# Kernel tuning notes

Hardware: AMD Instinct MI355X
Metric: run time of the kernel (lower is better)

## Reference

```python
import jax, jax.numpy as jnp
import numpy as np

NEG_SLOPE = 0.2  # LeakyReLU(0.2) used for attention scores


def setup_inputs() -> dict:
    key = jax.random.key(0)
    k1, k2, k3, k4, k5 = jax.random.split(key, 5)
    B, H, N, F, D = 1024, 32, 25, 128, 128
    return {
        "x_self": jax.random.normal(k1, (B, H, F), dtype=jnp.float32),
        "x_neigh": jax.random.normal(k2, (B, H, N, F), dtype=jnp.float32),
        "w_feat": jax.random.normal(k3, (F, D), dtype=jnp.float32) * 0.1,
        "a_self": jax.random.normal(k4, (D, 1), dtype=jnp.float32) * 0.1,
        "a_neigh": jax.random.normal(k5, (D, 1), dtype=jnp.float32) * 0.1,
    }


def reference(x_self, x_neigh, w_feat, a_self, a_neigh):
    # xw_self: [B, H, 1, D]; xw_neigh: [B, H, N, D]
    xw_self = jnp.einsum("bhf,fd->bhd", x_self, w_feat)[:, :, None, :]
    xw_neigh = jnp.einsum("bhnf,fd->bhnd", x_neigh, w_feat)
    xw_all = jnp.concatenate([xw_self, xw_neigh], axis=2)  # [B, H, N+1, D]
    # attention scores over the (self + neighbours) axis
    attn_self = jnp.einsum("bhkd,do->bhko", xw_self, a_self)   # [B, H, 1, 1]
    attn_neigh = jnp.einsum("bhkd,do->bhko", xw_all, a_neigh)  # [B, H, N+1, 1]
    attn_u = jax.nn.leaky_relu(attn_self + attn_neigh, negative_slope=NEG_SLOPE)
    attn = jax.nn.softmax(attn_u, axis=2)                      # [B, H, N+1, 1]
    h_out = jnp.sum(attn * xw_all, axis=2)                     # [B, H, D]
    return jax.nn.relu(h_out)
```

## Files before the change

kernel.cpp:

```cpp
#include <hip/hip_runtime.h>

typedef unsigned short u16;
typedef unsigned int   u32;
typedef __attribute__((ext_vector_type(4))) float f32x4;
typedef __attribute__((ext_vector_type(4))) int   i32x4;
typedef __attribute__((ext_vector_type(4))) u32   u32x4;

#define NPAIR 32768
#define NB    25
#define FD    128

__device__ __forceinline__ float bflo(u32 u){ return __uint_as_float(u << 16); }
__device__ __forceinline__ float bfhi(u32 u){ return __uint_as_float(u & 0xFFFF0000u); }
__device__ __forceinline__ u16 f2bf(float f){
  u32 u = __float_as_uint(f);
  u += 0x7FFFu + ((u >> 16) & 1u);
  return (u16)(u >> 16);
}
__device__ __forceinline__ float rowsum16(float x){
  x += __shfl_xor(x, 1);
  x += __shfl_xor(x, 2);
  x += __shfl_xor(x, 4);
  x += __shfl_xor(x, 8);
  return x;
}
__device__ __forceinline__ bool sniff_f32(const u16* __restrict__ xsniff, int l){
  const u16 v1 = xsniff[l], v2 = xsniff[64 + l];
  int e1 = (v1 >> 7) & 0xFF, e2 = (v2 >> 7) & 0xFF;
  int e = e1 > e2 ? e1 : e2;
  #pragma unroll
  for (int m = 1; m <= 32; m <<= 1){ int o = __shfl_xor(e, m); e = e > o ? e : o; }
  unsigned long long zb = __ballot(((l & 1) == 0) && (v1 == 0 || v2 == 0));
  return (e >= 141) || (__popcll(zb) >= 20);
}

__global__ __launch_bounds__(64) void prep(const void* w_, const void* as_, const void* an_,
                                           const u16* __restrict__ xsniff,
                                           float* __restrict__ wa, u16* __restrict__ wpk,
                                           int* __restrict__ flag_out){
  const int l = threadIdx.x;
  const bool isf32 = sniff_f32(xsniff, l);

  if (blockIdx.x < FD){
    const int f = blockIdx.x;
    float ps, pn;
    if (isf32){
      const float* w  = (const float*)w_;
      const float* as = (const float*)as_;
      const float* an = (const float*)an_;
      float w0 = w[f*FD + 2*l], w1 = w[f*FD + 2*l + 1];
      ps = w0*as[2*l] + w1*as[2*l+1];
      pn = w0*an[2*l] + w1*an[2*l+1];
    } else {
      const u16* w  = (const u16*)w_;
      const u16* as = (const u16*)as_;
      const u16* an = (const u16*)an_;
      u32 wd = *(const u32*)(w + f*FD + 2*l);
      u32 av = *(const u32*)(as + 2*l);
      u32 nv = *(const u32*)(an + 2*l);
      ps = bflo(wd)*bflo(av) + bfhi(wd)*bfhi(av);
      pn = bflo(wd)*bflo(nv) + bfhi(wd)*bfhi(nv);
    }
    #pragma unroll
    for(int m=1; m<=32; m<<=1){ ps += __shfl_xor(ps, m); pn += __shfl_xor(pn, m); }
    if (l == 0){ wa[f] = ps; wa[FD + f] = pn; }
    if (blockIdx.x == 0 && l == 0) flag_out[0] = isf32 ? 1 : 0;
  } else {
    const int unit = (blockIdx.x - FD)*64 + l;
    const int nt   = unit >> 8;
    const int kt   = (unit >> 6) & 3;
    const int fl   = unit & 63;
    const int col  = fl & 15, quad = fl >> 4;
    union { u16 s[8]; u32x4 u; } bb;
    #pragma unroll
    for (int j = 0; j < 8; ++j){
      const int idx = (kt*32 + quad*8 + j)*FD + nt*16 + col;
      bb.s[j] = isf32 ? f2bf(((const float*)w_)[idx]) : ((const u16*)w_)[idx];
    }
    *(u32x4*)(wpk + unit*8) = bb.u;
  }
}

template<bool FP32>
__device__ __forceinline__ void fused_body(const void* __restrict__ xs_, const void* __restrict__ xn_,
                                           const float* __restrict__ wa, const u16* __restrict__ wpk,
                                           void* __restrict__ out_, u16* __restrict__ xb){
  const int tid  = threadIdx.x;
  const int lane = tid & 63, wv = tid >> 6;
  const int g  = lane >> 4;
  const int q  = lane & 15;
  const int f0 = q << 3;
  const int pbase = blockIdx.x * 16;

  float was[8], wan[8];
  {
    f32x4 a = *(const f32x4*)(wa + f0);
    f32x4 b = *(const f32x4*)(wa + f0 + 4);
    was[0]=a[0]; was[1]=a[1]; was[2]=a[2]; was[3]=a[3];
    was[4]=b[0]; was[5]=b[1]; was[6]=b[2]; was[7]=b[3];
    f32x4 c = *(const f32x4*)(wa + FD + f0);
    f32x4 d = *(const f32x4*)(wa + FD + f0 + 4);
    wan[0]=c[0]; wan[1]=c[1]; wan[2]=c[2]; wan[3]=c[3];
    wan[4]=d[0]; wan[5]=d[1]; wan[6]=d[2]; wan[7]=d[3];
  }

  #pragma unroll 1
  for (int pp = 0; pp < 4; ++pp){
    const int row = wv*4 + pp;
    const int p   = pbase + row;

    float xf[7][8];
    #pragma unroll
    for(int i=0;i<7;++i){
      const int v = 4*i + g;
      if (v <= NB){
        if (FP32){
          const float* src = (v==0) ? ((const float*)xs_ + (size_t)p*FD + f0)
                                    : ((const float*)xn_ + (size_t)p*(NB*FD) + (size_t)(v-1)*FD + f0);
          f32x4 A = __builtin_nontemporal_load((const f32x4*)src);
          f32x4 B = __builtin_nontemporal_load((const f32x4*)(src + 4));
          xf[i][0]=A[0]; xf[i][1]=A[1]; xf[i][2]=A[2]; xf[i][3]=A[3];
          xf[i][4]=B[0]; xf[i][5]=B[1]; xf[i][6]=B[2]; xf[i][7]=B[3];
        } else {
          const u16* src = (v==0) ? ((const u16*)xs_ + (size_t)p*FD + f0)
                                  : ((const u16*)xn_ + (size_t)p*(NB*FD) + (size_t)(v-1)*FD + f0);
          u32x4 d = __builtin_nontemporal_load((const u32x4*)src);
          xf[i][0]=bflo(d[0]); xf[i][1]=bfhi(d[0]);
          xf[i][2]=bflo(d[1]); xf[i][3]=bfhi(d[1]);
          xf[i][4]=bflo(d[2]); xf[i][5]=bfhi(d[2]);
          xf[i][6]=bflo(d[3]); xf[i][7]=bfhi(d[3]);
        }
      } else {
        #pragma unroll
        for(int j=0;j<8;++j) xf[i][j] = 0.f;
      }
    }

    float pn[7];
    #pragma unroll
    for(int i=0;i<7;++i){
      float s = 0.f;
      #pragma unroll
      for(int j=0;j<8;++j) s += xf[i][j]*wan[j];
      pn[i] = rowsum16(s);
    }
    float ps = 0.f;
    #pragma unroll
    for(int j=0;j<8;++j) ps += xf[0][j]*was[j];
    ps = rowsum16(ps);
    const float s_self = __shfl(ps, 0);

    float u[7];
    #pragma unroll
    for(int i=0;i<7;++i){
      const int v = 4*i + g;
      if (v <= NB){
        float t = s_self + pn[i];
        u[i] = fmaxf(t, 0.2f*t);
      } else u[i] = -3.0e38f;
    }
    float m = u[0];
    #pragma unroll
    for(int i=1;i<7;++i) m = fmaxf(m, u[i]);
    m = fmaxf(m, __shfl_xor(m, 16));
    m = fmaxf(m, __shfl_xor(m, 32));

    float e[7]; float S = 0.f;
    #pragma unroll
    for(int i=0;i<7;++i){
      const int v = 4*i + g;
      e[i] = (v <= NB) ? __expf(u[i] - m) : 0.f;
      S += e[i];
    }
    S += __shfl_xor(S, 16);
    S += __shfl_xor(S, 32);
    const float rinv = 1.0f / S;

    float acc[8];
    #pragma unroll
    for(int j=0;j<8;++j) acc[j] = 0.f;
    #pragma unroll
    for(int i=0;i<7;++i)
      #pragma unroll
      for(int j=0;j<8;++j) acc[j] += e[i]*xf[i][j];
    #pragma unroll
    for(int j=0;j<8;++j){
      acc[j] += __shfl_xor(acc[j], 16);
      acc[j] += __shfl_xor(acc[j], 32);
      acc[j] *= rinv;
    }
    if (g == 0){
      u32 o0 = (u32)f2bf(acc[0]) | ((u32)f2bf(acc[1])<<16);
      u32 o1 = (u32)f2bf(acc[2]) | ((u32)f2bf(acc[3])<<16);
      u32 o2 = (u32)f2bf(acc[4]) | ((u32)f2bf(acc[5])<<16);
      u32 o3 = (u32)f2bf(acc[6]) | ((u32)f2bf(acc[7])<<16);
      u32x4 ov = {o0, o1, o2, o3};
      *(u32x4*)(xb + row*FD + f0) = ov;
    }
  }
  __syncthreads();

  const int col = q, quad = g;
  i32x4 bfru[2][4];
  #pragma unroll
  for (int ntl = 0; ntl < 2; ++ntl)
    #pragma unroll
    for (int kt = 0; kt < 4; ++kt)
      bfru[ntl][kt] = *(const i32x4*)(wpk + (size_t)(((wv*2 + ntl)*4 + kt)*64 + lane)*8);

  f32x4 acc2[2];
  { f32x4 z = {0.f,0.f,0.f,0.f}; acc2[0] = z; acc2[1] = z; }
  #pragma unroll
  for (int kt = 0; kt < 4; ++kt){
    i32x4 av = *(const i32x4*)(xb + col*FD + kt*32 + quad*8);
    #pragma unroll
    for (int ntl = 0; ntl < 2; ++ntl){
      asm volatile("s_nop 1\n\t"
                   "v_mfma_f32_16x16x32_bf16 %0, %1, %2, %0\n\t"
                   "s_nop 7\n\t"
                   "s_nop 7"
                   : "+v"(acc2[ntl]) : "v"(av), "v"(bfru[ntl][kt]));
    }
  }
  if (FP32){
    float* o = (float*)out_;
    #pragma unroll
    for (int ntl = 0; ntl < 2; ++ntl){
      const int n0 = (wv*2 + ntl)*16 + col;
      #pragma unroll
      for (int r = 0; r < 4; ++r)
        o[(size_t)(pbase + quad*4 + r)*FD + n0] = fmaxf(acc2[ntl][r], 0.f);
    }
  } else {
    u16* o = (u16*)out_;
    #pragma unroll
    for (int ntl = 0; ntl < 2; ++ntl){
      const int n0 = (wv*2 + ntl)*16 + col;
      #pragma unroll
      for (int r = 0; r < 4; ++r)
        o[(size_t)(pbase + quad*4 + r)*FD + n0] = f2bf(fmaxf(acc2[ntl][r], 0.f));
    }
  }
}

__global__ __launch_bounds__(256) void fused(const void* __restrict__ xs, const void* __restrict__ xn,
                                             const float* __restrict__ wa, const int* __restrict__ flag,
                                             const u16* __restrict__ wpk, void* __restrict__ out_){
  __shared__ u16 xb[16*FD];
  if (flag[0]) fused_body<true >(xs, xn, wa, wpk, out_, xb);
  else         fused_body<false>(xs, xn, wa, wpk, out_, xb);
}

extern "C" void kernel_launch(void* const* d_in, const int* in_sizes, int n_in,
                              void* d_out, int out_size, void* d_ws, size_t ws_size,
                              hipStream_t stream){
  const void* x_self  = d_in[0];
  const void* x_neigh = d_in[1];
  const void* w_feat  = d_in[2];
  const void* a_self  = d_in[3];
  const void* a_neigh = d_in[4];

  int*   flag = (int*)d_ws;
  float* wa   = (float*)d_ws + 64;
  u16*   wpk  = (u16*)d_ws + 1024;

  prep <<<FD + 32,  64, 0, stream>>>(w_feat, a_self, a_neigh, (const u16*)x_self, wa, wpk, flag);
  fused<<<NPAIR/16, 256, 0, stream>>>(x_self, x_neigh, wa, flag, wpk, d_out);
}
```

Measured before the change: 549.7 us.

## Double-buffer neighbour tiles into LDS with async global_load_lds prefetch

```diff
diff --git a/kernel.cpp b/kernel.cpp
--- a/kernel.cpp
+++ b/kernel.cpp
@@ -9,6 +9,7 @@
 #define NPAIR 32768
 #define NB    25
 #define FD    128
+#define TILEB 13312
 
 __device__ __forceinline__ float bflo(u32 u){ return __uint_as_float(u << 16); }
 __device__ __forceinline__ float bfhi(u32 u){ return __uint_as_float(u & 0xFFFF0000u); }
@@ -32,6 +33,48 @@
   for (int m = 1; m <= 32; m <<= 1){ int o = __shfl_xor(e, m); e = e > o ? e : o; }
   unsigned long long zb = __ballot(((l & 1) == 0) && (v1 == 0 || v2 == 0));
   return (e >= 141) || (__popcll(zb) >= 20);
+}
+
+__device__ __forceinline__ void gld16(const void* g, void* l){
+  __builtin_amdgcn_global_load_lds((const __attribute__((address_space(1))) u32*)g,
+                                   (__attribute__((address_space(3))) u32*)l, 16, 0, 0);
+}
+__device__ __forceinline__ void gld4(const void* g, void* l){
+  __builtin_amdgcn_global_load_lds((const __attribute__((address_space(1))) u32*)g,
+                                   (__attribute__((address_space(3))) u32*)l, 4, 0, 0);
+}
+template<int N> __device__ __forceinline__ void wait_vmcnt(){
+  if constexpr (N == 0)  asm volatile("s_waitcnt vmcnt(0)"  ::: "memory");
+  if constexpr (N == 8)  asm volatile("s_waitcnt vmcnt(8)"  ::: "memory");
+  if constexpr (N == 13) asm volatile("s_waitcnt vmcnt(13)" ::: "memory");
+  __builtin_amdgcn_sched_barrier(0);
+}
+
+template<bool FP32>
+__device__ __forceinline__ void stage_pair(const char* xs, const char* xn, int p, char* slot, int lane){
+  if constexpr (FP32){
+    #pragma unroll
+    for (int c = 0; c < 13; ++c){
+      const int o = c*1024 + lane*16;
+      const char* src = (o < 512) ? (xs + (size_t)p*512   + o)
+                                  : (xn + (size_t)p*12800 + (o - 512));
+      gld16(src, slot + c*1024);
+    }
+  } else {
+    #pragma unroll
+    for (int c = 0; c < 6; ++c){
+      const int o = c*1024 + lane*16;
+      const char* src = (o < 256) ? (xs + (size_t)p*256  + o)
+                                  : (xn + (size_t)p*6400 + (o - 256));
+      gld16(src, slot + c*1024);
+    }
+    #pragma unroll
+    for (int c = 0; c < 2; ++c){
+      const int o = 6144 + c*256 + lane*4;
+      const char* src = xn + (size_t)p*6400 + (o - 256);
+      gld4(src, slot + 6144 + c*256);
+    }
+  }
 }
 
 __global__ __launch_bounds__(64) void prep(const void* w_, const void* as_, const void* an_,
@@ -84,13 +127,16 @@
 template<bool FP32>
 __device__ __forceinline__ void fused_body(const void* __restrict__ xs_, const void* __restrict__ xn_,
                                            const float* __restrict__ wa, const u16* __restrict__ wpk,
-                                           void* __restrict__ out_, u16* __restrict__ xb){
+                                           void* __restrict__ out_, char* stg, u16* xb){
   const int tid  = threadIdx.x;
   const int lane = tid & 63, wv = tid >> 6;
   const int g  = lane >> 4;
   const int q  = lane & 15;
   const int f0 = q << 3;
   const int pbase = blockIdx.x * 16;
+  const int p0    = pbase + wv*4;
+  const char* xs = (const char*)xs_;
+  const char* xn = (const char*)xn_;
 
   float was[8], wan[8];
   {
@@ -104,27 +150,42 @@
     wan[4]=d[0]; wan[5]=d[1]; wan[6]=d[2]; wan[7]=d[3];
   }
 
-  #pragma unroll 1
+  i32x4 bfru[2][4];
+  #pragma unroll
+  for (int ntl = 0; ntl < 2; ++ntl)
+    #pragma unroll
+    for (int kt = 0; kt < 4; ++kt)
+      bfru[ntl][kt] = *(const i32x4*)(wpk + (size_t)(((wv*2 + ntl)*4 + kt)*64 + lane)*8);
+
+  char* slot0 = stg + (size_t)wv*TILEB;
+  char* slot1 = stg + (size_t)(4 + wv)*TILEB;
+  stage_pair<FP32>(xs, xn, p0, slot0, lane);
+
+  #pragma unroll
   for (int pp = 0; pp < 4; ++pp){
-    const int row = wv*4 + pp;
-    const int p   = pbase + row;
+    char* cur = (pp & 1) ? slot1 : slot0;
+    char* nxt = (pp & 1) ? slot0 : slot1;
+    if (pp < 3){
+      stage_pair<FP32>(xs, xn, p0 + pp + 1, nxt, lane);
+      wait_vmcnt<(FP32 ? 13 : 8)>();
+    } else {
+      wait_vmcnt<0>();
+    }
 
     float xf[7][8];
     #pragma unroll
     for(int i=0;i<7;++i){
       const int v = 4*i + g;
       if (v <= NB){
-        if (FP32){
-          const float* src = (v==0) ? ((const float*)xs_ + (size_t)p*FD + f0)
-                                    : ((const float*)xn_ + (size_t)p*(NB*FD) + (size_t)(v-1)*FD + f0);
-          f32x4 A = __builtin_nontemporal_load((const f32x4*)src);
-          f32x4 B = __builtin_nontemporal_load((const f32x4*)(src + 4));
+        if constexpr (FP32){
+          const char* rp = cur + v*512 + f0*4;
+          f32x4 A = *(const f32x4*)rp;
+          f32x4 B = *(const f32x4*)(rp + 16);
           xf[i][0]=A[0]; xf[i][1]=A[1]; xf[i][2]=A[2]; xf[i][3]=A[3];
           xf[i][4]=B[0]; xf[i][5]=B[1]; xf[i][6]=B[2]; xf[i][7]=B[3];
         } else {
-          const u16* src = (v==0) ? ((const u16*)xs_ + (size_t)p*FD + f0)
-                                  : ((const u16*)xn_ + (size_t)p*(NB*FD) + (size_t)(v-1)*FD + f0);
-          u32x4 d = __builtin_nontemporal_load((const u32x4*)src);
+          const char* rp = cur + v*256 + f0*2;
+          u32x4 d = *(const u32x4*)rp;
           xf[i][0]=bflo(d[0]); xf[i][1]=bfhi(d[0]);
           xf[i][2]=bflo(d[1]); xf[i][3]=bfhi(d[1]);
           xf[i][4]=bflo(d[2]); xf[i][5]=bfhi(d[2]);
@@ -190,6 +251,7 @@
       acc[j] *= rinv;
     }
     if (g == 0){
+      const int row = wv*4 + pp;
       u32 o0 = (u32)f2bf(acc[0]) | ((u32)f2bf(acc[1])<<16);
       u32 o1 = (u32)f2bf(acc[2]) | ((u32)f2bf(acc[3])<<16);
       u32 o2 = (u32)f2bf(acc[4]) | ((u32)f2bf(acc[5])<<16);
@@ -201,13 +263,6 @@
   __syncthreads();
 
   const int col = q, quad = g;
-  i32x4 bfru[2][4];
-  #pragma unroll
-  for (int ntl = 0; ntl < 2; ++ntl)
-    #pragma unroll
-    for (int kt = 0; kt < 4; ++kt)
-      bfru[ntl][kt] = *(const i32x4*)(wpk + (size_t)(((wv*2 + ntl)*4 + kt)*64 + lane)*8);
-
   f32x4 acc2[2];
   { f32x4 z = {0.f,0.f,0.f,0.f}; acc2[0] = z; acc2[1] = z; }
   #pragma unroll
@@ -243,12 +298,13 @@
   }
 }
 
-__global__ __launch_bounds__(256) void fused(const void* __restrict__ xs, const void* __restrict__ xn,
-                                             const float* __restrict__ wa, const int* __restrict__ flag,
-                                             const u16* __restrict__ wpk, void* __restrict__ out_){
-  __shared__ u16 xb[16*FD];
-  if (flag[0]) fused_body<true >(xs, xn, wa, wpk, out_, xb);
-  else         fused_body<false>(xs, xn, wa, wpk, out_, xb);
+__global__ __launch_bounds__(256, 1) void fused(const void* __restrict__ xs, const void* __restrict__ xn,
+                                                const float* __restrict__ wa, const int* __restrict__ flag,
+                                                const u16* __restrict__ wpk, void* __restrict__ out_){
+  __shared__ __align__(16) char stg[8*TILEB];
+  __shared__ __align__(16) u16  xb[16*FD];
+  if (flag[0]) fused_body<true >(xs, xn, wa, wpk, out_, stg, xb);
+  else         fused_body<false>(xs, xn, wa, wpk, out_, stg, xb);
 }
 
 extern "C" void kernel_launch(void* const* d_in, const int* in_sizes, int n_in,
```

Result: slower. 572.0 us (+4.0%).
